# Optimization experiments

Hardware: AMD Instinct MI355X
Metric: run time of the kernel (lower is better)

The kernel has to match this reference:

```python
import jax, jax.numpy as jnp
import numpy as np

N = 50000
E = 800000
IN_DIM = 256
H1, D1 = 4, 128   # layer1: 4 heads x 128 = 512 concat
H2, D2 = 1, 256   # layer2: 1 head x 256
NEG_SLOPE = 0.2


def setup_inputs() -> dict:
    key = jax.random.key(0)
    ks = jax.random.split(key, 12)
    feat = jax.random.normal(ks[0], (N, IN_DIM), dtype=jnp.float32)
    src1 = jax.random.randint(ks[1], (E,), 0, N)
    dst1 = jax.random.randint(ks[2], (E,), 0, N)
    src2 = jax.random.randint(ks[3], (E,), 0, N)
    dst2 = jax.random.randint(ks[4], (E,), 0, N)
    s1 = 1.0 / np.sqrt(IN_DIM)
    s2 = 1.0 / np.sqrt(H1 * D1)
    W1 = jax.random.normal(ks[5], (IN_DIM, H1 * D1), dtype=jnp.float32) * s1
    al1 = jax.random.normal(ks[6], (H1, D1), dtype=jnp.float32) * s1
    ar1 = jax.random.normal(ks[7], (H1, D1), dtype=jnp.float32) * s1
    W2 = jax.random.normal(ks[8], (H1 * D1, H2 * D2), dtype=jnp.float32) * s2
    al2 = jax.random.normal(ks[9], (H2, D2), dtype=jnp.float32) * s2
    ar2 = jax.random.normal(ks[10], (H2, D2), dtype=jnp.float32) * s2
    return {"feat": feat, "src1": src1, "dst1": dst1, "src2": src2,
            "dst2": dst2, "W1": W1, "al1": al1, "ar1": ar1,
            "W2": W2, "al2": al2, "ar2": ar2}


def gat_layer(x, W, al, ar, src, dst, heads):
    n = x.shape[0]
    h = (x @ W).reshape(n, heads, -1)               # [N,H,D]
    el = jnp.einsum('nhd,hd->nh', h, al)            # attention left term
    er = jnp.einsum('nhd,hd->nh', h, ar)            # attention right term
    e = jax.nn.leaky_relu(el[src] + er[dst], NEG_SLOPE)   # [E,H]
    # segment softmax over edges grouped by destination node
    m = jax.ops.segment_max(e, dst, num_segments=n)
    m = jax.lax.stop_gradient(jnp.where(jnp.isfinite(m), m, 0.0))
    ee = jnp.exp(e - m[dst])
    s = jax.ops.segment_sum(ee, dst, num_segments=n)
    alpha = ee / (s[dst] + 1e-9)                    # [E,H]
    msg = h[src] * alpha[:, :, None]                # [E,H,D]
    return jax.ops.segment_sum(msg, dst, num_segments=n)  # [N,H,D]


def reference(feat, src1, dst1, src2, dst2, W1, al1, ar1, W2, al2, ar2):
    h1 = gat_layer(feat, W1, al1, ar1, src1, dst1, H1)      # [N,4,128]
    h1 = jax.nn.elu(h1.reshape(N, H1 * D1))                 # concat heads + act
    z = gat_layer(h1, W2, al2, ar2, src2, dst2, H2)         # [N,1,256]
    return z.reshape(N, D2)                                 # no act on last layer
```

## Files before the change

### kernel.cpp

```cpp
#include <hip/hip_runtime.h>
#include <stdint.h>

#define NN 50000
#define EE 800000
#define IND 256
#define HD1 512
#define D2C 256

#define NB1 782
#define NB  (2 * NB1)
#define CH  16384
#define WGN ((2 * EE + CH - 1) / CH)
#define TOT (NB * WGN)
#define SB2 ((TOT + 255) / 256)

#define Q_SCALE 21.166666f
#define Q_INV   0.047244094f

typedef float f32x4 __attribute__((ext_vector_type(4)));
typedef __bf16 bf16x8 __attribute__((ext_vector_type(8)));

__device__ inline float bf2f(unsigned int u) {
    union { unsigned int i; float f; } c; c.i = u << 16; return c.f;
}
__device__ inline unsigned int f2bf(float f) {
    union { float f; unsigned int i; } c; c.f = f;
    unsigned int x = c.i;
    return (x + 0x7FFFu + ((x >> 16) & 1u)) >> 16;
}
__device__ inline float loadf(const void* p, int idx, int isbf) {
    return isbf ? bf2f(((const unsigned short*)p)[idx]) : ((const float*)p)[idx];
}
__device__ inline unsigned int f2q8(float v) {
    float t = fminf(fmaxf(v * Q_SCALE, -127.f), 127.f);
    int q = (int)rintf(t) + 128;
    return (unsigned int)q & 0xFFu;
}
__device__ inline void unpack8_u8(uint2 q, float* o) {
    o[0] = (float)(q.x & 0xFFu);
    o[1] = (float)((q.x >> 8) & 0xFFu);
    o[2] = (float)((q.x >> 16) & 0xFFu);
    o[3] = (float)(q.x >> 24);
    o[4] = (float)(q.y & 0xFFu);
    o[5] = (float)((q.y >> 8) & 0xFFu);
    o[6] = (float)((q.y >> 16) & 0xFFu);
    o[7] = (float)(q.y >> 24);
}
__device__ inline void glds16(const unsigned short* g, unsigned short* lds_base) {
    __builtin_amdgcn_global_load_lds(
        (const __attribute__((address_space(1))) void*)g,
        (__attribute__((address_space(3))) void*)lds_base, 16, 0, 0);
}

__global__ void probe_k(const unsigned int* __restrict__ w, int* __restrict__ flag) {
    __shared__ int red[256];
    int t = threadIdx.x;
    int ok = 0;
    for (int i = t; i < 4096; i += 256) {
        unsigned int v = w[i];
        unsigned int e0 = (v >> 7) & 0xffu;
        unsigned int e1 = (v >> 23) & 0xffu;
        ok += (e0 <= 133u) + (e1 <= 133u);
    }
    red[t] = ok;
    __syncthreads();
    for (int s = 128; s > 0; s >>= 1) {
        if (t < s) red[t] += red[t + s];
        __syncthreads();
    }
    if (t == 0) *flag = (red[0] >= 7782) ? 1 : 0;
}

__global__ __launch_bounds__(256) void convert_k(
    const void* __restrict__ in, const int* __restrict__ flagp,
    unsigned short* __restrict__ out)
{
    int isbf = (*flagp != 0);
    size_t i = ((size_t)blockIdx.x * 256 + threadIdx.x) * 8;
    if (i >= (size_t)NN * IND) return;
    if (isbf) {
        *(uint4*)(out + i) = *(const uint4*)((const unsigned short*)in + i);
    } else {
        const float* f = (const float*)in + i;
        f32x4 p0 = *(const f32x4*)f;
        f32x4 p1 = *(const f32x4*)(f + 4);
        uint4 va;
        va.x = f2bf(p0.x) | (f2bf(p0.y) << 16);
        va.y = f2bf(p0.z) | (f2bf(p0.w) << 16);
        va.z = f2bf(p1.x) | (f2bf(p1.y) << 16);
        va.w = f2bf(p1.z) | (f2bf(p1.w) << 16);
        *(uint4*)(out + i) = va;
    }
}

__global__ __launch_bounds__(256) void gemm_bt(
    const unsigned short* __restrict__ A, const int* __restrict__ flagp,
    const unsigned short* __restrict__ BT,
    void* __restrict__ C, int c_q8,
    int M, int K, int Nc,
    const void* __restrict__ al, const void* __restrict__ ar,
    float* __restrict__ el, float* __restrict__ er, int eler_mode)
{
    __shared__ unsigned short Als[2][128 * 32];
    __shared__ unsigned short Bls[2][128 * 32];
    __shared__ float elp[128];
    __shared__ float erp[128];
    int isbf = (*flagp != 0);
    int tid  = threadIdx.x;
    int wave = tid >> 6;
    int lane = tid & 63;
    int wr = (wave >> 1) * 64;
    int wc = (wave & 1) * 64;
    int m0 = blockIdx.x * 128;
    int n0 = blockIdx.y * 128;
    if (tid < 128) { elp[tid] = 0.f; erp[tid] = 0.f; }
    f32x4 acc[4][4];
#pragma unroll
    for (int i = 0; i < 4; i++)
#pragma unroll
        for (int j = 0; j < 4; j++) acc[i][j] = (f32x4){0.f, 0.f, 0.f, 0.f};
    int frow = lane & 15;
    int kg = (lane >> 4) * 8;
    int srow = lane >> 2;
    int scol = (lane & 3) * 8;
    auto STAGE = [&](int buf, int kt) {
#pragma unroll
        for (int q = 0; q < 2; ++q) {
            int chunk = wave + q * 4;
            int r = chunk * 16 + srow;
            int gm = m0 + r; if (gm >= M) gm = M - 1;
            glds16(A + (size_t)gm * K + kt + scol, Als[buf] + chunk * 512);
            glds16(BT + (size_t)(n0 + r) * K + kt + scol, Bls[buf] + chunk * 512);
        }
    };
    int nt = K >> 5;
    int cur = 0;
    STAGE(0, 0);
    __syncthreads();
    for (int t = 0; t < nt; ++t) {
        if (t + 1 < nt) STAGE(cur ^ 1, (t + 1) * 32);
        bf16x8 af[4], bfr[4];
#pragma unroll
        for (int i = 0; i < 4; i++)
            af[i] = __builtin_bit_cast(bf16x8, *(const uint4*)(Als[cur] + (wr + i * 16 + frow) * 32 + kg));
#pragma unroll
        for (int j = 0; j < 4; j++)
            bfr[j] = __builtin_bit_cast(bf16x8, *(const uint4*)(Bls[cur] + (wc + j * 16 + frow) * 32 + kg));
#pragma unroll
        for (int i = 0; i < 4; i++)
#pragma unroll
            for (int j = 0; j < 4; j++)
                acc[i][j] = __builtin_amdgcn_mfma_f32_16x16x32_bf16(af[i], bfr[j], acc[i][j], 0, 0, 0);
        __syncthreads();
        cur ^= 1;
    }
    int nb = n0 + wc + frow;
    int mb = m0 + wr + (lane >> 4) * 4;
#pragma unroll
    for (int i = 0; i < 4; i++) {
#pragma unroll
        for (int j = 0; j < 4; j++) {
            int n = nb + j * 16;
#pragma unroll
            for (int r = 0; r < 4; r++) {
                int m = mb + i * 16 + r;
                if (m < M) {
                    if (c_q8)
                        ((unsigned char*)C)[(size_t)m * Nc + n] = (unsigned char)f2q8(acc[i][j][r]);
                    else
                        ((unsigned short*)C)[(size_t)m * Nc + n] = (unsigned short)f2bf(acc[i][j][r]);
                }
            }
        }
    }
    float alv[4], arv[4];
#pragma unroll
    for (int j = 0; j < 4; j++) {
        int c = n0 + wc + frow + j * 16;
        alv[j] = loadf(al, c, isbf);
        arv[j] = loadf(ar, c, isbf);
    }
#pragma unroll
    for (int i = 0; i < 4; i++) {
#pragma unroll
        for (int r = 0; r < 4; r++) {
            float pe = 0.f, pr = 0.f;
#pragma unroll
            for (int j = 0; j < 4; j++) {
                pe += acc[i][j][r] * alv[j];
                pr += acc[i][j][r] * arv[j];
            }
#pragma unroll
            for (int o = 1; o < 16; o <<= 1) {
                pe += __shfl_xor(pe, o);
                pr += __shfl_xor(pr, o);
            }
            if ((lane & 15) == 0) {
                int row = wr + (lane >> 4) * 4 + i * 16 + r;
                atomicAdd(&elp[row], pe);
                atomicAdd(&erp[row], pr);
            }
        }
    }
    __syncthreads();
    if (tid < 128) {
        int m = m0 + tid;
        if (m < M) {
            if (eler_mode == 1) {
                el[m * 4 + blockIdx.y] = elp[tid];
                er[m * 4 + blockIdx.y] = erp[tid];
            } else {
                atomicAdd(&el[m], elp[tid]);
                atomicAdd(&er[m], erp[tid]);
            }
        }
    }
}

__global__ void transpose_k(const void* __restrict__ in, const int* __restrict__ flagp,
                            unsigned short* __restrict__ out, int R, int C) {
    int isbf = (*flagp != 0);
    int idx = blockIdx.x * blockDim.x + threadIdx.x;
    if (idx < R * C) {
        int i = idx / C, j = idx - i * C;
        unsigned short v = isbf ? ((const unsigned short*)in)[idx]
                                : (unsigned short)f2bf(((const float*)in)[idx]);
        out[j * R + i] = v;
    }
}

__global__ __launch_bounds__(256) void binA_k(
    const int* __restrict__ dst1, const int* __restrict__ dst2,
    int* __restrict__ hist)
{
    __shared__ int lh[NB];
    int t = threadIdx.x, w = blockIdx.x;
    for (int b = t; b < NB; b += 256) lh[b] = 0;
    __syncthreads();
    int base = w * CH;
    for (int k = 0; k < CH; k += 256) {
        int i = base + k + t;
        if (i < 2 * EE) {
            int d, lay;
            if (i < EE) { d = dst1[i]; lay = 0; }
            else        { d = dst2[i - EE]; lay = 1; }
            d = ((unsigned)d < (unsigned)NN) ? d : 0;
            atomicAdd(&lh[lay * NB1 + (d >> 6)], 1);
        }
    }
    __syncthreads();
    for (int b = t; b < NB; b += 256) hist[b * WGN + w] = lh[b];
}
__global__ void scan_a(int* __restrict__ hist, int* __restrict__ bsum) {
    __shared__ int sdata[256];
    int t = threadIdx.x;
    int g = blockIdx.x * 256 + t;
    int v = (g < TOT) ? hist[g] : 0;
    sdata[t] = v;
    __syncthreads();
    for (int o = 1; o < 256; o <<= 1) {
        int x = (t >= o) ? sdata[t - o] : 0;
        __syncthreads();
        sdata[t] += x;
        __syncthreads();
    }
    if (g < TOT) hist[g] = sdata[t] - v;
    if (t == 255) bsum[blockIdx.x] = sdata[255];
}
__global__ void scan_b(const int* __restrict__ bsum, int* __restrict__ boff) {
    __shared__ int sdata[1024];
    int t = threadIdx.x;
    int v = (t < SB2) ? bsum[t] : 0;
    sdata[t] = v;
    __syncthreads();
    for (int o = 1; o < 1024; o <<= 1) {
        int x = (t >= o) ? sdata[t - o] : 0;
        __syncthreads();
        sdata[t] += x;
        __syncthreads();
    }
    boff[t] = sdata[t] - v;
}
__global__ void scan_c(int* __restrict__ hist, const int* __restrict__ boff) {
    int g = blockIdx.x * 256 + threadIdx.x;
    if (g < TOT) hist[g] += boff[blockIdx.x];
}
__global__ __launch_bounds__(256) void binC_k(
    const int* __restrict__ src1, const int* __restrict__ dst1,
    const int* __restrict__ src2, const int* __restrict__ dst2,
    const int* __restrict__ base_g, unsigned int* __restrict__ bucketed)
{
    __shared__ int cur[NB];
    int t = threadIdx.x, w = blockIdx.x;
    for (int b = t; b < NB; b += 256) cur[b] = base_g[b * WGN + w];
    __syncthreads();
    int base = w * CH;
    for (int k = 0; k < CH; k += 256) {
        int i = base + k + t;
        if (i < 2 * EE) {
            int d, s, lay;
            if (i < EE) { d = dst1[i]; s = src1[i]; lay = 0; }
            else        { d = dst2[i - EE]; s = src2[i - EE]; lay = 1; }
            d = ((unsigned)d < (unsigned)NN) ? d : 0;
            s = ((unsigned)s < (unsigned)NN) ? s : 0;
            int b = lay * NB1 + (d >> 6);
            int p = atomicAdd(&cur[b], 1);
            bucketed[p] = (unsigned)s | ((unsigned)(d & 63) << 16);
        }
    }
}
__global__ __launch_bounds__(256) void binD_k(
    const int* __restrict__ base_g, const unsigned int* __restrict__ bucketed,
    int* __restrict__ csr, int* __restrict__ row_ptr)
{
    __shared__ int cnt[64];
    __shared__ int off[64];
    __shared__ int cur[64];
    int b = blockIdx.x, t = threadIdx.x;
    int s = base_g[b * WGN];
    int e = (b + 1 < NB) ? base_g[(b + 1) * WGN] : (2 * EE);
    int lay = (b >= NB1) ? 1 : 0;
    int b0 = b - lay * NB1;
    if (t < 64) cnt[t] = 0;
    __syncthreads();
    for (int i = s + t; i < e; i += 256)
        atomicAdd(&cnt[bucketed[i] >> 16], 1);
    __syncthreads();
    if (t == 0) {
        int run = s;
        for (int j = 0; j < 64; j++) { off[j] = run; run += cnt[j]; }
    }
    __syncthreads();
    if (t < 64) {
        int node = b0 * 64 + t;
        if (node < NN) row_ptr[lay * NN + node] = off[t];
        cur[t] = off[t];
    }
    __syncthreads();
    for (int i = s + t; i < e; i += 256) {
        unsigned v = bucketed[i];
        int p = atomicAdd(&cur[v >> 16], 1);
        unsigned node = (unsigned)(b0 * 64) + (v >> 16);
        csr[p] = (int)((v & 0xFFFFu) | (node << 16));
    }
    if (b == NB - 1 && t == 0) row_ptr[2 * NN] = e;
}

__global__ __launch_bounds__(256) void wgt1_k(
    const int* __restrict__ csr, const float* __restrict__ el,
    const float* __restrict__ er, float* __restrict__ w)
{
    int idx = blockIdx.x * 256 + threadIdx.x;
    if (idx >= EE * 4) return;
    int p = idx >> 2, h = idx & 3;
    unsigned c = (unsigned)csr[p];
    int s = (int)(c & 0xFFFFu);
    int d = (int)(c >> 16);
    s = ((unsigned)s < (unsigned)NN) ? s : 0;
    d = ((unsigned)d < (unsigned)NN) ? d : 0;
    float ev = el[s * 4 + h] + er[d * 4 + h];
    ev = (ev > 0.f) ? ev : 0.2f * ev;
    w[idx] = __expf(fminf(ev, 80.f));
}
__global__ __launch_bounds__(256) void wgt2_k(
    const int* __restrict__ csr, const float* __restrict__ el,
    const float* __restrict__ er, float* __restrict__ w)
{
    int p = blockIdx.x * 256 + threadIdx.x;
    if (p >= EE) return;
    unsigned c = (unsigned)csr[EE + p];
    int s = (int)(c & 0xFFFFu);
    int d = (int)(c >> 16);
    s = ((unsigned)s < (unsigned)NN) ? s : 0;
    d = ((unsigned)d < (unsigned)NN) ? d : 0;
    float ev = el[s] + er[d];
    ev = (ev > 0.f) ? ev : 0.2f * ev;
    w[p] = __expf(fminf(ev, 80.f));
}

__global__ __launch_bounds__(256) void agg1_k(
    const unsigned char* __restrict__ h1,
    const float* __restrict__ wgt,
    const int* __restrict__ row_ptr, const int* __restrict__ csr,
    unsigned short* __restrict__ x2)
{
    int wv = (blockIdx.x * blockDim.x + threadIdx.x) >> 6;
    int lane = threadIdx.x & 63;
    if (wv >= NN) return;
    int h = lane >> 4;
    int e0 = row_ptr[wv], e1 = row_ptr[wv + 1];
    float l = 0.f;
    float acc[8];
#pragma unroll
    for (int j = 0; j < 8; j++) acc[j] = 0.f;
    int e = e0;
    for (; e + 3 < e1; e += 4) {
        int c0 = csr[e],     c1 = csr[e + 1];
        int c2 = csr[e + 2], c3 = csr[e + 3];
        int s0 = c0 & 0xFFFF, s1 = c1 & 0xFFFF;
        int s2 = c2 & 0xFFFF, s3 = c3 & 0xFFFF;
        s0 = ((unsigned)s0 < (unsigned)NN) ? s0 : 0;
        s1 = ((unsigned)s1 < (unsigned)NN) ? s1 : 0;
        s2 = ((unsigned)s2 < (unsigned)NN) ? s2 : 0;
        s3 = ((unsigned)s3 < (unsigned)NN) ? s3 : 0;
        uint2 p0 = *(const uint2*)(h1 + (size_t)s0 * HD1 + lane * 8);
        uint2 p1 = *(const uint2*)(h1 + (size_t)s1 * HD1 + lane * 8);
        uint2 p2 = *(const uint2*)(h1 + (size_t)s2 * HD1 + lane * 8);
        uint2 p3 = *(const uint2*)(h1 + (size_t)s3 * HD1 + lane * 8);
        float w0 = wgt[e * 4 + h];
        float w1 = wgt[(e + 1) * 4 + h];
        float w2 = wgt[(e + 2) * 4 + h];
        float w3 = wgt[(e + 3) * 4 + h];
        float f0[8], f1[8], f2[8], f3[8];
        unpack8_u8(p0, f0);
        unpack8_u8(p1, f1);
        unpack8_u8(p2, f2);
        unpack8_u8(p3, f3);
        l += (w0 + w1) + (w2 + w3);
#pragma unroll
        for (int j = 0; j < 8; j++)
            acc[j] += (w0 * f0[j] + w1 * f1[j]) + (w2 * f2[j] + w3 * f3[j]);
    }
    for (; e < e1; ++e) {
        int s = csr[e] & 0xFFFF;
        s = ((unsigned)s < (unsigned)NN) ? s : 0;
        float w0 = wgt[e * 4 + h];
        l += w0;
        float hf[8];
        unpack8_u8(*(const uint2*)(h1 + (size_t)s * HD1 + lane * 8), hf);
#pragma unroll
        for (int j = 0; j < 8; j++) acc[j] += w0 * hf[j];
    }
    float inv = 1.f / (l + 1e-9f);
    float sc = Q_INV * inv;
    float bias = 128.f * l;
    unsigned int o[4];
#pragma unroll
    for (int j = 0; j < 4; j++) {
        float v0 = (acc[2 * j] - bias) * sc;
        float v1 = (acc[2 * j + 1] - bias) * sc;
        v0 = (v0 > 0.f) ? v0 : (__expf(v0) - 1.f);
        v1 = (v1 > 0.f) ? v1 : (__expf(v1) - 1.f);
        o[j] = f2bf(v0) | (f2bf(v1) << 16);
    }
    *(uint4*)(x2 + (size_t)wv * HD1 + lane * 8) = make_uint4(o[0], o[1], o[2], o[3]);
}

__global__ __launch_bounds__(256) void agg2_k(
    const unsigned short* __restrict__ h2,
    const float* __restrict__ wgt,
    const int* __restrict__ row_ptr, const int* __restrict__ csr,
    void* __restrict__ outv, const int* __restrict__ flagp)
{
    int isbf = (*flagp != 0);
    int wv = (blockIdx.x * blockDim.x + threadIdx.x) >> 6;
    int lane = threadIdx.x & 63;
    if (wv >= NN) return;
    int e0 = row_ptr[NN + wv], e1 = row_ptr[NN + wv + 1];
    float l = 0.f;
    float a0 = 0.f, a1 = 0.f, a2 = 0.f, a3 = 0.f;
    int e = e0;
    for (; e + 3 < e1; e += 4) {
        int c0 = csr[e],     c1 = csr[e + 1];
        int c2 = csr[e + 2], c3 = csr[e + 3];
        int s0 = c0 & 0xFFFF, s1 = c1 & 0xFFFF;
        int s2 = c2 & 0xFFFF, s3 = c3 & 0xFFFF;
        s0 = ((unsigned)s0 < (unsigned)NN) ? s0 : 0;
        s1 = ((unsigned)s1 < (unsigned)NN) ? s1 : 0;
        s2 = ((unsigned)s2 < (unsigned)NN) ? s2 : 0;
        s3 = ((unsigned)s3 < (unsigned)NN) ? s3 : 0;
        uint2 t0 = *(const uint2*)(h2 + (size_t)s0 * D2C + lane * 4);
        uint2 t1 = *(const uint2*)(h2 + (size_t)s1 * D2C + lane * 4);
        uint2 t2 = *(const uint2*)(h2 + (size_t)s2 * D2C + lane * 4);
        uint2 t3 = *(const uint2*)(h2 + (size_t)s3 * D2C + lane * 4);
        float w0 = wgt[e - EE];
        float w1 = wgt[e + 1 - EE];
        float w2 = wgt[e + 2 - EE];
        float w3 = wgt[e + 3 - EE];
        l += (w0 + w1) + (w2 + w3);
        a0 += (w0 * bf2f(t0.x & 0xffffu) + w1 * bf2f(t1.x & 0xffffu))
            + (w2 * bf2f(t2.x & 0xffffu) + w3 * bf2f(t3.x & 0xffffu));
        a1 += (w0 * bf2f(t0.x >> 16)     + w1 * bf2f(t1.x >> 16))
            + (w2 * bf2f(t2.x >> 16)     + w3 * bf2f(t3.x >> 16));
        a2 += (w0 * bf2f(t0.y & 0xffffu) + w1 * bf2f(t1.y & 0xffffu))
            + (w2 * bf2f(t2.y & 0xffffu) + w3 * bf2f(t3.y & 0xffffu));
        a3 += (w0 * bf2f(t0.y >> 16)     + w1 * bf2f(t1.y >> 16))
            + (w2 * bf2f(t2.y >> 16)     + w3 * bf2f(t3.y >> 16));
    }
    for (; e < e1; ++e) {
        int s = csr[e] & 0xFFFF;
        s = ((unsigned)s < (unsigned)NN) ? s : 0;
        float w0 = wgt[e - EE];
        l += w0;
        uint2 t = *(const uint2*)(h2 + (size_t)s * D2C + lane * 4);
        a0 += w0 * bf2f(t.x & 0xffffu);
        a1 += w0 * bf2f(t.x >> 16);
        a2 += w0 * bf2f(t.y & 0xffffu);
        a3 += w0 * bf2f(t.y >> 16);
    }
    float inv = 1.f / (l + 1e-9f);
    float v0 = a0 * inv, v1 = a1 * inv, v2 = a2 * inv, v3 = a3 * inv;
    if (isbf) {
        uint2 o;
        o.x = f2bf(v0) | (f2bf(v1) << 16);
        o.y = f2bf(v2) | (f2bf(v3) << 16);
        *(uint2*)((unsigned short*)outv + (size_t)wv * D2C + lane * 4) = o;
    } else {
        f32x4 o = (f32x4){v0, v1, v2, v3};
        *(f32x4*)((float*)outv + (size_t)wv * D2C + lane * 4) = o;
    }
}

extern "C" void kernel_launch(void* const* d_in, const int* in_sizes, int n_in,
                              void* d_out, int out_size, void* d_ws, size_t ws_size,
                              hipStream_t stream) {
    const void* feat = d_in[0];
    const int* src1 = (const int*)d_in[1];
    const int* dst1 = (const int*)d_in[2];
    const int* src2 = (const int*)d_in[3];
    const int* dst2 = (const int*)d_in[4];
    const void* W1  = d_in[5];
    const void* al1 = d_in[6];
    const void* ar1 = d_in[7];
    const void* W2  = d_in[8];
    const void* al2 = d_in[9];
    const void* ar2 = d_in[10];

    uint8_t* w = (uint8_t*)d_ws;
    auto alloc = [&](size_t bytes) -> void* {
        void* p = (void*)w;
        w += (bytes + 255) & ~(size_t)255;
        return p;
    };
    int* flag    = (int*)alloc(256);
    float* el    = (float*)alloc((size_t)NN * 4 * 4);
    float* er    = (float*)alloc((size_t)NN * 4 * 4);
    unsigned short* W1T = (unsigned short*)alloc((size_t)IND * HD1 * 2);
    unsigned short* W2T = (unsigned short*)alloc((size_t)HD1 * D2C * 2);
    int* hist    = (int*)alloc((size_t)TOT * 4);
    int* bsum    = (int*)alloc(1024 * 4);
    int* boff    = (int*)alloc(1024 * 4);
    unsigned int* bucketed = (unsigned int*)alloc((size_t)2 * EE * 4);
    int* csr     = (int*)alloc((size_t)2 * EE * 4);
    int* row_ptr = (int*)alloc((size_t)(2 * NN + 1) * 4);
    unsigned char* h1 = (unsigned char*)alloc((size_t)NN * HD1);
    unsigned short* x2 = (unsigned short*)alloc((size_t)NN * HD1 * 2);
    float* w1e   = (float*)alloc((size_t)EE * 4 * 4);
    unsigned short* h2 = (unsigned short*)h1;
    unsigned short* featb = x2;
    float* w2e   = (float*)bucketed;

    probe_k<<<1, 256, 0, stream>>>((const unsigned int*)feat, flag);
    convert_k<<<(NN * IND / 8 + 255) / 256, 256, 0, stream>>>(feat, flag, featb);
    transpose_k<<<(IND * HD1 + 255) / 256, 256, 0, stream>>>(W1, flag, W1T, IND, HD1);
    transpose_k<<<(HD1 * D2C + 255) / 256, 256, 0, stream>>>(W2, flag, W2T, HD1, D2C);

    binA_k<<<WGN, 256, 0, stream>>>(dst1, dst2, hist);
    scan_a<<<SB2, 256, 0, stream>>>(hist, bsum);
    scan_b<<<1, 1024, 0, stream>>>(bsum, boff);
    scan_c<<<SB2, 256, 0, stream>>>(hist, boff);
    binC_k<<<WGN, 256, 0, stream>>>(src1, dst1, src2, dst2, hist, bucketed);
    binD_k<<<NB, 256, 0, stream>>>(hist, bucketed, csr, row_ptr);

    gemm_bt<<<dim3((NN + 127) / 128, HD1 / 128), 256, 0, stream>>>(
        featb, flag, W1T, h1, 1, NN, IND, HD1, al1, ar1, el, er, 1);
    wgt1_k<<<(EE * 4 + 255) / 256, 256, 0, stream>>>(csr, el, er, w1e);
    agg1_k<<<(NN + 3) / 4, 256, 0, stream>>>(h1, w1e, row_ptr, csr, x2);

    hipMemsetAsync(el, 0, (size_t)NN * 4, stream);
    hipMemsetAsync(er, 0, (size_t)NN * 4, stream);
    gemm_bt<<<dim3((NN + 127) / 128, D2C / 128), 256, 0, stream>>>(
        x2, flag, W2T, (void*)h2, 0, NN, HD1, D2C, al2, ar2, el, er, 2);
    wgt2_k<<<(EE + 255) / 256, 256, 0, stream>>>(csr, el, er, w2e);
    agg2_k<<<(NN + 3) / 4, 256, 0, stream>>>(h2, w2e, row_ptr, csr, d_out, flag);
}
```

Before: 454.6 us.

## Load GEMM MFMA fragments directly from global memory instead of LDS staging

```diff
diff --git a/kernel.cpp b/kernel.cpp
--- a/kernel.cpp
+++ b/kernel.cpp
@@ -45,11 +45,6 @@
     o[5] = (float)((q.y >> 8) & 0xFFu);
     o[6] = (float)((q.y >> 16) & 0xFFu);
     o[7] = (float)(q.y >> 24);
-}
-__device__ inline void glds16(const unsigned short* g, unsigned short* lds_base) {
-    __builtin_amdgcn_global_load_lds(
-        (const __attribute__((address_space(1))) void*)g,
-        (__attribute__((address_space(3))) void*)lds_base, 16, 0, 0);
 }
 
 __global__ void probe_k(const unsigned int* __restrict__ w, int* __restrict__ flag) {
@@ -101,8 +96,6 @@
     const void* __restrict__ al, const void* __restrict__ ar,
     float* __restrict__ el, float* __restrict__ er, int eler_mode)
 {
-    __shared__ unsigned short Als[2][128 * 32];
-    __shared__ unsigned short Bls[2][128 * 32];
     __shared__ float elp[128];
     __shared__ float erp[128];
     int isbf = (*flagp != 0);
@@ -121,38 +114,29 @@
         for (int j = 0; j < 4; j++) acc[i][j] = (f32x4){0.f, 0.f, 0.f, 0.f};
     int frow = lane & 15;
     int kg = (lane >> 4) * 8;
-    int srow = lane >> 2;
-    int scol = (lane & 3) * 8;
-    auto STAGE = [&](int buf, int kt) {
-#pragma unroll
-        for (int q = 0; q < 2; ++q) {
-            int chunk = wave + q * 4;
-            int r = chunk * 16 + srow;
-            int gm = m0 + r; if (gm >= M) gm = M - 1;
-            glds16(A + (size_t)gm * K + kt + scol, Als[buf] + chunk * 512);
-            glds16(BT + (size_t)(n0 + r) * K + kt + scol, Bls[buf] + chunk * 512);
-        }
-    };
-    int nt = K >> 5;
-    int cur = 0;
-    STAGE(0, 0);
-    __syncthreads();
-    for (int t = 0; t < nt; ++t) {
-        if (t + 1 < nt) STAGE(cur ^ 1, (t + 1) * 32);
+    const unsigned short* Ap[4];
+    const unsigned short* Bp[4];
+#pragma unroll
+    for (int i = 0; i < 4; i++) {
+        int gm = m0 + wr + i * 16 + frow;
+        if (gm >= M) gm = M - 1;
+        Ap[i] = A + (size_t)gm * K + kg;
+        Bp[i] = BT + (size_t)(n0 + wc + i * 16 + frow) * K + kg;
+    }
+#pragma unroll 2
+    for (int kt = 0; kt < K; kt += 32) {
         bf16x8 af[4], bfr[4];
 #pragma unroll
         for (int i = 0; i < 4; i++)
-            af[i] = __builtin_bit_cast(bf16x8, *(const uint4*)(Als[cur] + (wr + i * 16 + frow) * 32 + kg));
+            af[i] = __builtin_bit_cast(bf16x8, *(const uint4*)(Ap[i] + kt));
 #pragma unroll
         for (int j = 0; j < 4; j++)
-            bfr[j] = __builtin_bit_cast(bf16x8, *(const uint4*)(Bls[cur] + (wc + j * 16 + frow) * 32 + kg));
+            bfr[j] = __builtin_bit_cast(bf16x8, *(const uint4*)(Bp[j] + kt));
 #pragma unroll
         for (int i = 0; i < 4; i++)
 #pragma unroll
             for (int j = 0; j < 4; j++)
                 acc[i][j] = __builtin_amdgcn_mfma_f32_16x16x32_bf16(af[i], bfr[j], acc[i][j], 0, 0, 0);
-        __syncthreads();
-        cur ^= 1;
     }
     int nb = n0 + wc + frow;
     int mb = m0 + wr + (lane >> 4) * 4;
@@ -180,6 +164,7 @@
         alv[j] = loadf(al, c, isbf);
         arv[j] = loadf(ar, c, isbf);
     }
+    __syncthreads();
 #pragma unroll
     for (int i = 0; i < 4; i++) {
 #pragma unroll
```

Measured after the change: 495.1 us. +8.9%, slower.

## Widen GEMM tile to 128x256 with 8 waves, drop el/er memsets and atomics

Applied to the files above, without the earlier changes.

```diff
diff --git a/kernel.cpp b/kernel.cpp
--- a/kernel.cpp
+++ b/kernel.cpp
@@ -93,7 +93,7 @@
     }
 }
 
-__global__ __launch_bounds__(256) void gemm_bt(
+__global__ __launch_bounds__(512) void gemm_bt(
     const unsigned short* __restrict__ A, const int* __restrict__ flagp,
     const unsigned short* __restrict__ BT,
     void* __restrict__ C, int c_q8,
@@ -102,18 +102,19 @@
     float* __restrict__ el, float* __restrict__ er, int eler_mode)
 {
     __shared__ unsigned short Als[2][128 * 32];
-    __shared__ unsigned short Bls[2][128 * 32];
-    __shared__ float elp[128];
-    __shared__ float erp[128];
+    __shared__ unsigned short Bls[2][256 * 32];
+    __shared__ float elp[2][128];
+    __shared__ float erp[2][128];
     int isbf = (*flagp != 0);
     int tid  = threadIdx.x;
     int wave = tid >> 6;
     int lane = tid & 63;
-    int wr = (wave >> 1) * 64;
-    int wc = (wave & 1) * 64;
+    int wr = (wave >> 2) * 64;
+    int wc = (wave & 3) * 64;
+    int hh = (wave & 3) >> 1;
     int m0 = blockIdx.x * 128;
-    int n0 = blockIdx.y * 128;
-    if (tid < 128) { elp[tid] = 0.f; erp[tid] = 0.f; }
+    int n0 = blockIdx.y * 256;
+    if (tid < 256) { (&elp[0][0])[tid] = 0.f; (&erp[0][0])[tid] = 0.f; }
     f32x4 acc[4][4];
 #pragma unroll
     for (int i = 0; i < 4; i++)
@@ -125,12 +126,16 @@
     int scol = (lane & 3) * 8;
     auto STAGE = [&](int buf, int kt) {
 #pragma unroll
-        for (int q = 0; q < 2; ++q) {
-            int chunk = wave + q * 4;
-            int r = chunk * 16 + srow;
-            int gm = m0 + r; if (gm >= M) gm = M - 1;
-            glds16(A + (size_t)gm * K + kt + scol, Als[buf] + chunk * 512);
-            glds16(BT + (size_t)(n0 + r) * K + kt + scol, Bls[buf] + chunk * 512);
+        for (int q = 0; q < 3; ++q) {
+            int chunk = wave * 3 + q;
+            if (chunk < 8) {
+                int r = chunk * 16 + srow;
+                int gm = m0 + r; if (gm >= M) gm = M - 1;
+                glds16(A + (size_t)gm * K + kt + scol, Als[buf] + chunk * 512);
+            } else {
+                int r = (chunk - 8) * 16 + srow;
+                glds16(BT + (size_t)(n0 + r) * K + kt + scol, Bls[buf] + (chunk - 8) * 512);
+            }
         }
     };
     int nt = K >> 5;
@@ -197,21 +202,22 @@
             }
             if ((lane & 15) == 0) {
                 int row = wr + (lane >> 4) * 4 + i * 16 + r;
-                atomicAdd(&elp[row], pe);
-                atomicAdd(&erp[row], pr);
+                atomicAdd(&elp[hh][row], pe);
+                atomicAdd(&erp[hh][row], pr);
             }
         }
     }
     __syncthreads();
-    if (tid < 128) {
-        int m = m0 + tid;
+    if (tid < 256) {
+        int row = tid & 127, half = tid >> 7;
+        int m = m0 + row;
         if (m < M) {
             if (eler_mode == 1) {
-                el[m * 4 + blockIdx.y] = elp[tid];
-                er[m * 4 + blockIdx.y] = erp[tid];
-            } else {
-                atomicAdd(&el[m], elp[tid]);
-                atomicAdd(&er[m], erp[tid]);
+                el[m * 4 + blockIdx.y * 2 + half] = elp[half][row];
+                er[m * 4 + blockIdx.y * 2 + half] = erp[half][row];
+            } else if (half == 0) {
+                el[m] = elp[0][row] + elp[1][row];
+                er[m] = erp[0][row] + erp[1][row];
             }
         }
     }
@@ -562,14 +568,12 @@
     binC_k<<<WGN, 256, 0, stream>>>(src1, dst1, src2, dst2, hist, bucketed);
     binD_k<<<NB, 256, 0, stream>>>(hist, bucketed, csr, row_ptr);
 
-    gemm_bt<<<dim3((NN + 127) / 128, HD1 / 128), 256, 0, stream>>>(
+    gemm_bt<<<dim3((NN + 127) / 128, HD1 / 256), 512, 0, stream>>>(
         featb, flag, W1T, h1, 1, NN, IND, HD1, al1, ar1, el, er, 1);
     wgt1_k<<<(EE * 4 + 255) / 256, 256, 0, stream>>>(csr, el, er, w1e);
     agg1_k<<<(NN + 3) / 4, 256, 0, stream>>>(h1, w1e, row_ptr, csr, x2);
 
-    hipMemsetAsync(el, 0, (size_t)NN * 4, stream);
-    hipMemsetAsync(er, 0, (size_t)NN * 4, stream);
-    gemm_bt<<<dim3((NN + 127) / 128, D2C / 128), 256, 0, stream>>>(
+    gemm_bt<<<dim3((NN + 127) / 128, D2C / 256), 512, 0, stream>>>(
         x2, flag, W2T, (void*)h2, 0, NN, HD1, D2C, al2, ar2, el, er, 2);
     wgt2_k<<<(EE + 255) / 256, 256, 0, stream>>>(csr, el, er, w2e);
     agg2_k<<<(NN + 3) / 4, 256, 0, stream>>>(h2, w2e, row_ptr, csr, d_out, flag);
```

Result: faster. 427.7 us (-5.9%).
